# Kernel optimization log

Hardware: AMD Instinct MI355X
Metric: run time of the kernel (lower is better)

## Reference

```python
import jax, jax.numpy as jnp
import numpy as np

THRESH = 0.5
TAU = 0.5
GAMMA = 1.0
BETA = 0.9
A = 0.5
B = 0.5


def zif_spike(v):
    # ZIF surrogate: forward is hard threshold (v > 0).
    return (v > 0).astype(v.dtype)


def setup_inputs() -> dict:
    key = jax.random.key(0)
    x = jax.random.normal(key, (64, 8192, 100), dtype=jnp.float32)
    return {"x": x}


def reference(x):
    # x: [B, N, T]; scan over time with (mem, w) state kept per element.
    xt = jnp.moveaxis(x, 2, 0)  # [T, B, N]
    init_mem = jnp.zeros(xt.shape[1:], dtype=x.dtype)
    init_w = jnp.zeros(xt.shape[1:], dtype=x.dtype)

    def step(carry, x_t):
        mem, w = carry
        mem = mem * TAU + x_t - w
        spike = zif_spike(mem - THRESH)
        w = BETA * w + (1.0 - BETA) * (A * mem + B * spike)
        mem = mem - spike * THRESH  # soft reset
        return (mem, w), spike

    _, spikes = jax.lax.scan(step, (init_mem, init_w), xt)  # [T, B, N]
    return jnp.moveaxis(spikes, 0, 2)  # [B, N, T]
```

## Files before the change

### kernel.cpp

```cpp
#include <hip/hip_runtime.h>

#define T_STEPS 100
#define CHUNKS  25
#define TPB     256
#define EPB     256
#define SLICES  5
#define SF4     5
#define WSLOT   (64 * SF4)

typedef const __attribute__((address_space(1))) unsigned int g_u32;
typedef __attribute__((address_space(3))) unsigned int l_u32;

__global__ __launch_bounds__(TPB) void lif_kernel(const float* __restrict__ x,
                                                  float* __restrict__ out) {
#pragma clang fp contract(off)
    __shared__ float4 lds[2][EPB * SF4];

    const int tid  = threadIdx.x;
    const int lane = tid & 63;
    const int w    = tid >> 6;

    const float* __restrict__ xw =
        x + ((size_t)blockIdx.x * EPB + (size_t)w * 64) * T_STEPS;

    const float* src[SF4];
#pragma unroll
    for (int i = 0; i < SF4; ++i) {
        const int f = i * 64 + lane;
        const int e = f / SF4;
        const int c = f - e * SF4;
        src[i] = xw + e * T_STEPS + c * 4;
    }

#pragma unroll
    for (int i = 0; i < SF4; ++i)
        __builtin_amdgcn_global_load_lds(
            (g_u32*)src[i], (l_u32*)&lds[0][w * WSLOT + i * 64], 16, 0, 0);

    unsigned b0 = 0, b1 = 0, b2 = 0, b3 = 0;
    float mem = 0.0f, wreg = 0.0f;

#pragma unroll
    for (int s = 0; s < SLICES; ++s) {
        const int buf = s & 1;

        if (s + 1 < SLICES) {
#pragma unroll
            for (int i = 0; i < SF4; ++i)
                __builtin_amdgcn_global_load_lds(
                    (g_u32*)(src[i] + (s + 1) * 4 * SF4),
                    (l_u32*)&lds[buf ^ 1][w * WSLOT + i * 64], 16, 0, 0);
            asm volatile("s_waitcnt vmcnt(5)" ::: "memory");
        } else {
            asm volatile("s_waitcnt vmcnt(0)" ::: "memory");
        }
        __builtin_amdgcn_sched_barrier(0);

        float4 xv[SF4];
#pragma unroll
        for (int c = 0; c < SF4; ++c) xv[c] = lds[buf][tid * SF4 + c];

#pragma unroll
        for (int c = 0; c < SF4; ++c) {
            float xs[4] = {xv[c].x, xv[c].y, xv[c].z, xv[c].w};
#pragma unroll
            for (int j = 0; j < 4; ++j) {
                mem = (mem * 0.5f + xs[j]) - wreg;
                const bool fire = (mem - 0.5f) > 0.0f;
                const float spike = fire ? 1.0f : 0.0f;
                wreg = 0.9f * wreg + 0.1f * (0.5f * mem + 0.5f * spike);
                mem = mem - spike * 0.5f;
                const int t = s * 20 + c * 4 + j;
                const unsigned bit = fire ? 1u : 0u;
                if (t < 32)      b0 |= bit << t;
                else if (t < 64) b1 |= bit << (t - 32);
                else if (t < 96) b2 |= bit << (t - 64);
                else             b3 |= bit << (t - 96);
            }
        }
    }

    float4* __restrict__ ow =
        (float4*)out + ((size_t)blockIdx.x * EPB + (size_t)w * 64) * CHUNKS;
#pragma unroll
    for (int k = 0; k < CHUNKS; ++k) {
        const int f = k * 64 + lane;
        const int e = f / 25;
        const int c = f - e * 25;
        const int a = e << 2;
        const unsigned w0 = (unsigned)__builtin_amdgcn_ds_bpermute(a, (int)b0);
        const unsigned w1 = (unsigned)__builtin_amdgcn_ds_bpermute(a, (int)b1);
        const unsigned w2 = (unsigned)__builtin_amdgcn_ds_bpermute(a, (int)b2);
        const unsigned w3 = (unsigned)__builtin_amdgcn_ds_bpermute(a, (int)b3);
        const unsigned word = (c < 16) ? ((c < 8) ? w0 : w1)
                                       : ((c < 24) ? w2 : w3);
        const int sh = (c & 7) * 4;
        float4 sv;
        sv.x = ((word >> (sh + 0)) & 1u) ? 1.0f : 0.0f;
        sv.y = ((word >> (sh + 1)) & 1u) ? 1.0f : 0.0f;
        sv.z = ((word >> (sh + 2)) & 1u) ? 1.0f : 0.0f;
        sv.w = ((word >> (sh + 3)) & 1u) ? 1.0f : 0.0f;
        ow[f] = sv;
    }
}

extern "C" void kernel_launch(void* const* d_in, const int* in_sizes, int n_in,
                              void* d_out, int out_size, void* d_ws, size_t ws_size,
                              hipStream_t stream) {
    const float* x = (const float*)d_in[0];
    float* out = (float*)d_out;
    int n_elem = in_sizes[0] / T_STEPS;
    int grid = n_elem / EPB;

    lif_kernel<<<grid, TPB, 0, stream>>>(x, out);
}
```

Measured before the change: 358.8 us.

## Replace LDS-staged coalesced loads with direct per-thread register prefetch pipeline

Drops the LDS double buffer fed by global_load_lds and has each thread load its own element's 100 timesteps straight into registers as float4 groups. A three-group register rotation prefetches upcoming groups while the current one is consumed, and launch bounds request four blocks per CU. This removes LDS traffic and waitcnt synchronisation, but each thread now reads a 400-byte strided row, so the loads of a wavefront are not contiguous and coalescing is worse.

```diff
diff --git a/kernel.cpp b/kernel.cpp
--- a/kernel.cpp
+++ b/kernel.cpp
@@ -3,91 +3,73 @@
 #define T_STEPS 100
 #define CHUNKS  25
 #define TPB     256
-#define EPB     256
-#define SLICES  5
-#define SF4     5
-#define WSLOT   (64 * SF4)
+#define GF4     5
 
-typedef const __attribute__((address_space(1))) unsigned int g_u32;
-typedef __attribute__((address_space(3))) unsigned int l_u32;
-
-__global__ __launch_bounds__(TPB) void lif_kernel(const float* __restrict__ x,
-                                                  float* __restrict__ out) {
+__global__ __launch_bounds__(TPB, 4) void lif_kernel(const float* __restrict__ x,
+                                                     float* __restrict__ out) {
 #pragma clang fp contract(off)
-    __shared__ float4 lds[2][EPB * SF4];
-
     const int tid  = threadIdx.x;
     const int lane = tid & 63;
     const int w    = tid >> 6;
 
-    const float* __restrict__ xw =
-        x + ((size_t)blockIdx.x * EPB + (size_t)w * 64) * T_STEPS;
-
-    const float* src[SF4];
-#pragma unroll
-    for (int i = 0; i < SF4; ++i) {
-        const int f = i * 64 + lane;
-        const int e = f / SF4;
-        const int c = f - e * SF4;
-        src[i] = xw + e * T_STEPS + c * 4;
-    }
-
-#pragma unroll
-    for (int i = 0; i < SF4; ++i)
-        __builtin_amdgcn_global_load_lds(
-            (g_u32*)src[i], (l_u32*)&lds[0][w * WSLOT + i * 64], 16, 0, 0);
+    const size_t e = (size_t)blockIdx.x * TPB + (size_t)tid;
+    const float4* __restrict__ xr = (const float4*)x + e * CHUNKS;
 
     unsigned b0 = 0, b1 = 0, b2 = 0, b3 = 0;
     float mem = 0.0f, wreg = 0.0f;
 
-#pragma unroll
-    for (int s = 0; s < SLICES; ++s) {
-        const int buf = s & 1;
+#define LOADG(G, g)                                                   \
+    do {                                                              \
+        _Pragma("unroll")                                             \
+        for (int i = 0; i < GF4; ++i) G[i] = xr[(g) * GF4 + i];       \
+    } while (0)
 
-        if (s + 1 < SLICES) {
-#pragma unroll
-            for (int i = 0; i < SF4; ++i)
-                __builtin_amdgcn_global_load_lds(
-                    (g_u32*)(src[i] + (s + 1) * 4 * SF4),
-                    (l_u32*)&lds[buf ^ 1][w * WSLOT + i * 64], 16, 0, 0);
-            asm volatile("s_waitcnt vmcnt(5)" ::: "memory");
-        } else {
-            asm volatile("s_waitcnt vmcnt(0)" ::: "memory");
-        }
-        __builtin_amdgcn_sched_barrier(0);
+#define CONSUME(G, s)                                                       \
+    do {                                                                    \
+        _Pragma("unroll")                                                   \
+        for (int c = 0; c < GF4; ++c) {                                     \
+            float xs[4] = {G[c].x, G[c].y, G[c].z, G[c].w};                 \
+            _Pragma("unroll")                                               \
+            for (int j = 0; j < 4; ++j) {                                   \
+                mem = (mem * 0.5f + xs[j]) - wreg;     \
+                const bool fire = (mem - 0.5f) > 0.0f;     \
+                const float spike = fire ? 1.0f : 0.0f;                     \
+                wreg = 0.9f * wreg + 0.1f * (0.5f * mem + 0.5f * spike);    \
+                mem = mem - spike * 0.5f;                   \
+                const int t = (s) * 20 + c * 4 + j;       \
+                const unsigned bit = fire ? 1u : 0u;                        \
+                if (t < 32)      b0 |= bit << t;                            \
+                else if (t < 64) b1 |= bit << (t - 32);                     \
+                else if (t < 96) b2 |= bit << (t - 64);                     \
+                else             b3 |= bit << (t - 96);                     \
+            }                                                               \
+        }                                                                   \
+    } while (0)
 
-        float4 xv[SF4];
-#pragma unroll
-        for (int c = 0; c < SF4; ++c) xv[c] = lds[buf][tid * SF4 + c];
+    float4 GA[GF4], GB[GF4], GC[GF4];
+    LOADG(GA, 0);
+    LOADG(GB, 1);
+    LOADG(GC, 2);
 
-#pragma unroll
-        for (int c = 0; c < SF4; ++c) {
-            float xs[4] = {xv[c].x, xv[c].y, xv[c].z, xv[c].w};
-#pragma unroll
-            for (int j = 0; j < 4; ++j) {
-                mem = (mem * 0.5f + xs[j]) - wreg;
-                const bool fire = (mem - 0.5f) > 0.0f;
-                const float spike = fire ? 1.0f : 0.0f;
-                wreg = 0.9f * wreg + 0.1f * (0.5f * mem + 0.5f * spike);
-                mem = mem - spike * 0.5f;
-                const int t = s * 20 + c * 4 + j;
-                const unsigned bit = fire ? 1u : 0u;
-                if (t < 32)      b0 |= bit << t;
-                else if (t < 64) b1 |= bit << (t - 32);
-                else if (t < 96) b2 |= bit << (t - 64);
-                else             b3 |= bit << (t - 96);
-            }
-        }
-    }
+    CONSUME(GA, 0);
+    LOADG(GA, 3);
+    CONSUME(GB, 1);
+    LOADG(GB, 4);
+    CONSUME(GC, 2);
+    CONSUME(GA, 3);
+    CONSUME(GB, 4);
+
+#undef LOADG
+#undef CONSUME
 
     float4* __restrict__ ow =
-        (float4*)out + ((size_t)blockIdx.x * EPB + (size_t)w * 64) * CHUNKS;
+        (float4*)out + ((size_t)blockIdx.x * TPB + (size_t)w * 64) * CHUNKS;
 #pragma unroll
     for (int k = 0; k < CHUNKS; ++k) {
         const int f = k * 64 + lane;
-        const int e = f / 25;
-        const int c = f - e * 25;
-        const int a = e << 2;
+        const int el = f / 25;
+        const int c  = f - el * 25;
+        const int a  = el << 2;
         const unsigned w0 = (unsigned)__builtin_amdgcn_ds_bpermute(a, (int)b0);
         const unsigned w1 = (unsigned)__builtin_amdgcn_ds_bpermute(a, (int)b1);
         const unsigned w2 = (unsigned)__builtin_amdgcn_ds_bpermute(a, (int)b2);
@@ -110,7 +92,7 @@
     const float* x = (const float*)d_in[0];
     float* out = (float*)d_out;
     int n_elem = in_sizes[0] / T_STEPS;
-    int grid = n_elem / EPB;
+    int grid = n_elem / TPB;
 
     lif_kernel<<<grid, TPB, 0, stream>>>(x, out);
 }
```

New measurement: 364.6 us. No clear change (+1.6%).
